# Optimization experiments

Hardware: AMD Instinct MI355X
Metric: run time of the kernel (lower is better)

The kernel has to match this reference:

```python
import jax, jax.numpy as jnp
import numpy as np

V, D, H, L, DF = 32000, 768, 12, 12, 3072
B, S, BS = 2, 1024, 16
MASK_ID = V - 1
HD = D // H
STD = 0.02


def setup_inputs() -> dict:
    key = jax.random.key(0)
    ks = jax.random.split(key, 12)
    ids = jax.random.randint(ks[0], (B, S), 0, V)
    m = jax.random.uniform(ks[1], (B, S)) < 0.15
    input_ids = jnp.where(m, MASK_ID, ids)
    target_ids = jax.random.randint(ks[2], (B, S), 0, V)
    noise_level = jax.random.uniform(ks[3], (B,), minval=0.1, maxval=1.0)
    emb = jax.random.normal(ks[4], (V, D)) * STD
    in_w = jax.random.normal(ks[5], (L, 3 * D, D)) * STD
    in_b = jnp.zeros((L, 3 * D))
    attn_out_w = jax.random.normal(ks[6], (L, D, D)) * STD
    attn_out_b = jnp.zeros((L, D))
    ln1_w = jnp.ones((L, D)); ln1_b = jnp.zeros((L, D))
    ln2_w = jnp.ones((L, D)); ln2_b = jnp.zeros((L, D))
    w1 = jax.random.normal(ks[7], (L, DF, D)) * STD; b1 = jnp.zeros((L, DF))
    w2 = jax.random.normal(ks[8], (L, D, DF)) * STD; b2 = jnp.zeros((L, D))
    proj_w = jax.random.normal(ks[9], (V, D)) * STD; proj_b = jnp.zeros((V,))
    return dict(input_ids=input_ids, target_ids=target_ids, noise_level=noise_level,
                emb=emb, in_w=in_w, in_b=in_b, attn_out_w=attn_out_w, attn_out_b=attn_out_b,
                ln1_w=ln1_w, ln1_b=ln1_b, ln2_w=ln2_w, ln2_b=ln2_b,
                w1=w1, b1=b1, w2=w2, b2=b2, proj_w=proj_w, proj_b=proj_b)


def _ln(x, w, b):
    m = x.mean(-1, keepdims=True)
    v = ((x - m) ** 2).mean(-1, keepdims=True)
    return (x - m) / jnp.sqrt(v + 1e-5) * w + b


def _rotary(x):
    # Vectorized equivalent of the per-scalar torch loop: rotates pairs
    # (0,1),(2,3),... within the first rotary_dim = D//2 channels only.
    rd = D // 2
    freqs = 1.0 / (10000.0 ** (jnp.arange(0, rd, 2, dtype=jnp.float32) / rd))  # [rd//2]
    ang = jnp.arange(S, dtype=jnp.float32)[:, None] * freqs[None, :]           # [S, rd//2]
    cos, sin = jnp.cos(ang), jnp.sin(ang)
    xr = x[..., :rd].reshape(B, S, rd // 2, 2)
    x0, x1 = xr[..., 0], xr[..., 1]
    r0 = x0 * cos - x1 * sin
    r1 = x0 * sin + x1 * cos
    rot = jnp.stack([r0, r1], axis=-1).reshape(B, S, rd)
    return jnp.concatenate([rot, x[..., rd:]], axis=-1)


def _block_causal_mask():
    nb = S // BS
    bm = jnp.tril(jnp.ones((nb, nb), dtype=jnp.float32))
    em = jnp.repeat(jnp.repeat(bm, BS, axis=0), BS, axis=1)  # [S, S]
    return (1.0 - em) * -1e9


def _model(input_ids, target_ids, noise_level, emb, in_w, in_b, attn_out_w, attn_out_b,
           ln1_w, ln1_b, ln2_w, ln2_b, w1, b1, w2, b2, proj_w, proj_b):
    x = emb[input_ids]                 # [B, S, D]
    x = _rotary(x)
    mask = _block_causal_mask()        # [S, S] additive
    scale = 1.0 / jnp.sqrt(jnp.float32(HD))
    for l in range(L):
        h = _ln(x, ln1_w[l], ln1_b[l])
        qkv = h @ in_w[l].T + in_b[l]
        q, k, v = jnp.split(qkv, 3, axis=-1)
        q = q.reshape(B, S, H, HD).transpose(0, 2, 1, 3)
        k = k.reshape(B, S, H, HD).transpose(0, 2, 1, 3)
        v = v.reshape(B, S, H, HD).transpose(0, 2, 1, 3)
        scores = jnp.einsum('bhqd,bhkd->bhqk', q, k) * scale + mask
        a = jax.nn.softmax(scores, axis=-1)
        o = jnp.einsum('bhqk,bhkd->bhqd', a, v).transpose(0, 2, 1, 3).reshape(B, S, D)
        x = x + (o @ attn_out_w[l].T + attn_out_b[l])
        h = _ln(x, ln2_w[l], ln2_b[l])
        x = x + (jax.nn.gelu(h @ w1[l].T + b1[l], approximate=False) @ w2[l].T + b2[l])
    logits = x @ proj_w.T + proj_b     # [B, S, V]
    logp = jax.nn.log_softmax(logits, axis=-1)
    ce = -jnp.take_along_axis(logp, target_ids[..., None], axis=-1)[..., 0]  # [B, S]
    is_masked = (input_ids == MASK_ID).astype(logits.dtype)
    weighted = ce * is_masked / noise_level[:, None]
    loss = weighted.sum() / (is_masked.sum() + 1e-8)
    return loss, logits


def reference(input_ids, target_ids, noise_level, emb, in_w, in_b, attn_out_w, attn_out_b,
              ln1_w, ln1_b, ln2_w, ln2_b, w1, b1, w2, b2, proj_w, proj_b):
    return _model(input_ids, target_ids, noise_level, emb, in_w, in_b, attn_out_w, attn_out_b,
                  ln1_w, ln1_b, ln2_w, ln2_b, w1, b1, w2, b2, proj_w, proj_b)
```

## Files before the change

### kernel.cpp

```cpp
#include <hip/hip_runtime.h>
#include <hip/hip_bf16.h>
#include <math.h>

#define V_SZ 32000
#define D_SZ 768
#define H_SZ 12
#define L_SZ 12
#define DF_SZ 3072
#define B_SZ 2
#define S_SZ 1024
#define BS_SZ 16
#define HD_SZ 64
#define MASK_ID 31999
#define NTOK (B_SZ * S_SZ)

typedef __attribute__((ext_vector_type(8))) short bf16x8;
typedef __attribute__((ext_vector_type(4))) short bf16x4;
typedef __attribute__((ext_vector_type(4))) float f32x4;

union B8 { bf16x8 v; __hip_bfloat162 h[4]; };
union B4 { bf16x4 v; __hip_bfloat162 h[2]; };
union U4 { ushort4 u; __hip_bfloat162 h[2]; };
union U4E { ushort4 u; unsigned short e[4]; };

__device__ inline unsigned short f2bf(float x) {
    __hip_bfloat16 b = __float2bfloat16(x);
    union { __hip_bfloat16 b; unsigned short u; } c; c.b = b;
    return c.u;
}

__global__ __launch_bounds__(256) void conv_fold_kernel(
    const float* __restrict__ Wsrc, const float* __restrict__ lnw,
    const float* __restrict__ lnb, const float* __restrict__ bsrc,
    unsigned short* __restrict__ Wdst, float* __restrict__ bdst,
    int rows_per_layer)
{
    const int gw = (blockIdx.x * 256 + threadIdx.x) >> 6;
    const int lane = threadIdx.x & 63;
    const int l = gw / rows_per_layer;
    const float* src = Wsrc + (size_t)gw * D_SZ;
    const float* wv = lnw + l * D_SZ;
    const float* bv = lnb + l * D_SZ;
    unsigned short* dst = Wdst + (size_t)gw * D_SZ;
    float acc = 0.f;
#pragma unroll
    for (int j = 0; j < 3; ++j) {
        int k = lane * 4 + j * 256;
        float4 s = *(const float4*)(src + k);
        float4 w = *(const float4*)(wv + k);
        float4 bb = *(const float4*)(bv + k);
        acc += bb.x * s.x + bb.y * s.y + bb.z * s.z + bb.w * s.w;
        U4 o;
        o.h[0] = __float22bfloat162_rn(float2{s.x * w.x, s.y * w.y});
        o.h[1] = __float22bfloat162_rn(float2{s.z * w.z, s.w * w.w});
        *(ushort4*)(dst + k) = o.u;
    }
#pragma unroll
    for (int off = 32; off; off >>= 1) acc += __shfl_xor(acc, off);
    if (lane == 0) bdst[gw] = bsrc[gw] + acc;
}

__global__ __launch_bounds__(256) void conv_cast_kernel(
    const float* __restrict__ src, unsigned short* __restrict__ dst, int n8)
{
    int i = blockIdx.x * 256 + threadIdx.x;
    if (i >= n8) return;
    const float* p = src + (size_t)i * 8;
    float4 v0 = *(const float4*)p;
    float4 v1 = *(const float4*)(p + 4);
    B8 r;
    r.h[0] = __float22bfloat162_rn(float2{v0.x, v0.y});
    r.h[1] = __float22bfloat162_rn(float2{v0.z, v0.w});
    r.h[2] = __float22bfloat162_rn(float2{v1.x, v1.y});
    r.h[3] = __float22bfloat162_rn(float2{v1.z, v1.w});
    *(bf16x8*)(dst + (size_t)i * 8) = r.v;
}

__global__ __launch_bounds__(256) void embed_rot_kernel(
    const int* __restrict__ ids, const float* __restrict__ emb,
    float* __restrict__ x)
{
    const int tok = blockIdx.x;
    const int s = tok & (S_SZ - 1);
    const int id = ids[tok];
    const float* e = emb + (size_t)id * D_SZ;
    float* xo = x + (size_t)tok * D_SZ;
    const int t = threadIdx.x;

    if (t < 192) {
        float x0 = e[2 * t], x1 = e[2 * t + 1];
        float freq = powf(10000.f, -((float)(2 * t)) / 384.f);
        float ang = (float)s * freq;
        float sn, cs;
        sincosf(ang, &sn, &cs);
        xo[2 * t]     = x0 * cs - x1 * sn;
        xo[2 * t + 1] = x0 * sn + x1 * cs;
    }
    for (int ch = 384 + t; ch < D_SZ; ch += 256) xo[ch] = e[ch];
}

template<int BM, int BN, int AM, int CM, bool WB16, bool XSWZ, bool CEP>
__global__ __launch_bounds__(256) void mfma_gemm(
    const void* __restrict__ Av, const void* __restrict__ Wv,
    const float* __restrict__ bias, const float* __restrict__ Res,
    float* __restrict__ C,
    unsigned short* __restrict__ qp, unsigned short* __restrict__ kp,
    unsigned short* __restrict__ vp, float2* __restrict__ pm,
    int M, int N, int K)
{
    constexpr int LDST = 48;
    constexpr int MR = BM / 32;
    constexpr int NR = BN / 32;
    constexpr int ACH = BM * 4 / 256;
    constexpr int BCH = BN * 4 / 256;

    __shared__ __align__(16) unsigned short As[2][BM * LDST];
    __shared__ __align__(16) unsigned short Bs[2][BN * LDST];
    __shared__ float smean[AM == 1 ? BM : 1];
    __shared__ float srstd[AM == 1 ? BM : 1];

    const int tid = threadIdx.x;
    const int lane = tid & 63;
    const int wave = tid >> 6;
    const int wrow0 = (wave >> 1) * (BM / 2);
    const int wcol0 = (wave & 1) * (BN / 2);
    const int kgrp = lane >> 4;
    const int rc = lane & 15;

    int m0, n0;
    if constexpr (XSWZ) {
        int nwg = gridDim.x * gridDim.y;
        int id = blockIdx.y * gridDim.x + blockIdx.x;
        int cpx = nwg >> 3;
        int swz = (id & 7) * cpx + (id >> 3);
        m0 = (swz % gridDim.x) * BM;
        n0 = (swz / gridDim.x) * BN;
    } else {
        m0 = blockIdx.x * BM;
        n0 = blockIdx.y * BN;
    }

    if constexpr (AM == 1) {
        const float* A = (const float*)Av;
        const int row = tid >> 2, q = tid & 3;
        const float* xr = A + (size_t)(m0 + row) * K + q * (K >> 2);
        float sum = 0.f, ss = 0.f;
        for (int j = 0; j < (K >> 4); ++j) {
            float4 v = *(const float4*)(xr + j * 4);
            sum += v.x + v.y + v.z + v.w;
            ss += v.x * v.x + v.y * v.y + v.z * v.z + v.w * v.w;
        }
        sum += __shfl_xor(sum, 1); sum += __shfl_xor(sum, 2);
        ss  += __shfl_xor(ss, 1);  ss  += __shfl_xor(ss, 2);
        float mean = sum * (1.f / (float)K);
        float var = ss * (1.f / (float)K) - mean * mean;
        if (q == 0) { smean[row] = mean; srstd[row] = rsqrtf(var + 1e-5f); }
        __syncthreads();
    }

    f32x4 acc[MR][NR];
#pragma unroll
    for (int i = 0; i < MR; ++i)
#pragma unroll
        for (int j = 0; j < NR; ++j) acc[i][j] = (f32x4){0.f, 0.f, 0.f, 0.f};

    float areg_0[AM != 2 ? ACH : 1][8], areg_1[AM != 2 ? ACH : 1][8];
    bf16x8 areg16_0[AM == 2 ? ACH : 1], areg16_1[AM == 2 ? ACH : 1];
    float bregf_0[WB16 ? 1 : BCH][8], bregf_1[WB16 ? 1 : BCH][8];
    bf16x8 breg16_0[WB16 ? BCH : 1], breg16_1[WB16 ? BCH : 1];

#define STAGE_LOAD(ST, K0) do {                                              \
    const int k0_ = (K0);                                                    \
    _Pragma("unroll")                                                        \
    for (int i_ = 0; i_ < ACH; ++i_) {                                       \
        int c_ = tid + i_ * 256;                                             \
        int row_ = c_ >> 2, ks_ = c_ & 3;                                    \
        if constexpr (AM == 2) {                                             \
            const unsigned short* A16_ = (const unsigned short*)Av;          \
            areg16_##ST[i_] = *(const bf16x8*)(A16_ + (size_t)(m0 + row_) * K + k0_ + ks_ * 8); \
        } else {                                                             \
            const float* Af_ = (const float*)Av;                             \
            const float* p_ = Af_ + (size_t)(m0 + row_) * K + k0_ + ks_ * 8; \
            float4 v0_ = *(const float4*)p_;                                 \
            float4 v1_ = *(const float4*)(p_ + 4);                           \
            areg_##ST[i_][0] = v0_.x; areg_##ST[i_][1] = v0_.y;              \
            areg_##ST[i_][2] = v0_.z; areg_##ST[i_][3] = v0_.w;              \
            areg_##ST[i_][4] = v1_.x; areg_##ST[i_][5] = v1_.y;              \
            areg_##ST[i_][6] = v1_.z; areg_##ST[i_][7] = v1_.w;              \
        }                                                                    \
    }                                                                        \
    _Pragma("unroll")                                                        \
    for (int i_ = 0; i_ < BCH; ++i_) {                                       \
        int c_ = tid + i_ * 256;                                             \
        int row_ = c_ >> 2, ks_ = c_ & 3;                                    \
        if constexpr (WB16) {                                                \
            const unsigned short* W16_ = (const unsigned short*)Wv;          \
            breg16_##ST[i_] = *(const bf16x8*)(W16_ + (size_t)(n0 + row_) * K + k0_ + ks_ * 8); \
        } else {                                                             \
            const float* Wf_ = (const float*)Wv;                             \
            const float* p_ = Wf_ + (size_t)(n0 + row_) * K + k0_ + ks_ * 8; \
            float4 v0_ = *(const float4*)p_;                                 \
            float4 v1_ = *(const float4*)(p_ + 4);                           \
            bregf_##ST[i_][0] = v0_.x; bregf_##ST[i_][1] = v0_.y;            \
            bregf_##ST[i_][2] = v0_.z; bregf_##ST[i_][3] = v0_.w;            \
            bregf_##ST[i_][4] = v1_.x; bregf_##ST[i_][5] = v1_.y;            \
            bregf_##ST[i_][6] = v1_.z; bregf_##ST[i_][7] = v1_.w;            \
        }                                                                    \
    }                                                                        \
} while (0)

#define STAGE_WRITE(ST, BUF) do {                                            \
    _Pragma("unroll")                                                        \
    for (int i_ = 0; i_ < ACH; ++i_) {                                       \
        int c_ = tid + i_ * 256;                                             \
        int row_ = c_ >> 2, ks_ = c_ & 3;                                    \
        if constexpr (AM == 2) {                                             \
            *(bf16x8*)&As[BUF][row_ * LDST + ks_ * 8] = areg16_##ST[i_];     \
        } else {                                                             \
            float sc_ = 1.f, sh_ = 0.f;                                      \
            if constexpr (AM == 1) { sc_ = srstd[row_]; sh_ = -smean[row_] * sc_; } \
            B8 r_;                                                           \
            r_.h[0] = __float22bfloat162_rn(float2{fmaf(areg_##ST[i_][0], sc_, sh_), fmaf(areg_##ST[i_][1], sc_, sh_)}); \
            r_.h[1] = __float22bfloat162_rn(float2{fmaf(areg_##ST[i_][2], sc_, sh_), fmaf(areg_##ST[i_][3], sc_, sh_)}); \
            r_.h[2] = __float22bfloat162_rn(float2{fmaf(areg_##ST[i_][4], sc_, sh_), fmaf(areg_##ST[i_][5], sc_, sh_)}); \
            r_.h[3] = __float22bfloat162_rn(float2{fmaf(areg_##ST[i_][6], sc_, sh_), fmaf(areg_##ST[i_][7], sc_, sh_)}); \
            *(bf16x8*)&As[BUF][row_ * LDST + ks_ * 8] = r_.v;                \
        }                                                                    \
    }                                                                        \
    _Pragma("unroll")                                                        \
    for (int i_ = 0; i_ < BCH; ++i_) {                                       \
        int c_ = tid + i_ * 256;                                             \
        int row_ = c_ >> 2, ks_ = c_ & 3;                                    \
        if constexpr (WB16) {                                                \
            *(bf16x8*)&Bs[BUF][row_ * LDST + ks_ * 8] = breg16_##ST[i_];     \
        } else {                                                             \
            B8 r_;                                                           \
            r_.h[0] = __float22bfloat162_rn(float2{bregf_##ST[i_][0], bregf_##ST[i_][1]}); \
            r_.h[1] = __float22bfloat162_rn(float2{bregf_##ST[i_][2], bregf_##ST[i_][3]}); \
            r_.h[2] = __float22bfloat162_rn(float2{bregf_##ST[i_][4], bregf_##ST[i_][5]}); \
            r_.h[3] = __float22bfloat162_rn(float2{bregf_##ST[i_][6], bregf_##ST[i_][7]}); \
            *(bf16x8*)&Bs[BUF][row_ * LDST + ks_ * 8] = r_.v;                \
        }                                                                    \
    }                                                                        \
} while (0)

#define COMPUTE(BUF) do {                                                    \
    bf16x8 af_[MR], bf_[NR];                                                 \
    _Pragma("unroll")                                                        \
    for (int mi_ = 0; mi_ < MR; ++mi_)                                       \
        af_[mi_] = *(const bf16x8*)&As[BUF][(wrow0 + mi_ * 16 + rc) * LDST + kgrp * 8]; \
    _Pragma("unroll")                                                        \
    for (int ni_ = 0; ni_ < NR; ++ni_)                                       \
        bf_[ni_] = *(const bf16x8*)&Bs[BUF][(wcol0 + ni_ * 16 + rc) * LDST + kgrp * 8]; \
    _Pragma("unroll")                                                        \
    for (int mi_ = 0; mi_ < MR; ++mi_)                                       \
        _Pragma("unroll")                                                    \
        for (int ni_ = 0; ni_ < NR; ++ni_)                                   \
            acc[mi_][ni_] = __builtin_amdgcn_mfma_f32_16x16x32_bf16(         \
                af_[mi_], bf_[ni_], acc[mi_][ni_], 0, 0, 0);                 \
} while (0)

    const int nk = K >> 5;
    STAGE_LOAD(0, 0);
    STAGE_WRITE(0, 0);
    STAGE_LOAD(0, 32);
    __syncthreads();

    for (int s2 = 0; s2 < nk; s2 += 2) {
        if (s2 + 2 < nk) STAGE_LOAD(1, (s2 + 2) << 5);
        COMPUTE(0);
        if (s2 + 1 < nk) STAGE_WRITE(0, 1);
        __syncthreads();
        if (s2 + 3 < nk) STAGE_LOAD(0, (s2 + 3) << 5);
        COMPUTE(1);
        if (s2 + 2 < nk) STAGE_WRITE(1, 0);
        __syncthreads();
    }
#undef STAGE_LOAD
#undef STAGE_WRITE
#undef COMPUTE

#pragma unroll
    for (int mi = 0; mi < MR; ++mi) {
#pragma unroll
        for (int ni = 0; ni < NR; ++ni) {
            const int col = n0 + wcol0 + ni * 16 + rc;
            const int rbase = m0 + wrow0 + mi * 16 + kgrp * 4;
            float bv = bias ? bias[col] : 0.f;
            if constexpr (CM == 1) {
                const int region = col / 768;
                const int c768 = col - region * 768;
                const int hh = c768 >> 6, d = c768 & 63;
                const int bb = rbase >> 10, s0 = rbase & 1023;
                const int bh = bb * H_SZ + hh;
                if (region == 0) {
#pragma unroll
                    for (int i = 0; i < 4; ++i)
                        qp[((size_t)(bh << 10) + s0 + i) * 64 + d]
                            = f2bf((acc[mi][ni][i] + bv) * 0.125f);
                } else if (region == 1) {
#pragma unroll
                    for (int i = 0; i < 4; ++i)
                        kp[((size_t)(bh << 10) + s0 + i) * 64 + d]
                            = f2bf(acc[mi][ni][i] + bv);
                } else {
                    U4E t4;
#pragma unroll
                    for (int i = 0; i < 4; ++i) t4.e[i] = f2bf(acc[mi][ni][i] + bv);
                    *(ushort4*)&vp[(((size_t)bh * 64 + d) << 10) + s0] = t4.u;
                }
            } else if constexpr (CM == 2) {
                unsigned short* C16 = (unsigned short*)C;
#pragma unroll
                for (int i = 0; i < 4; ++i) {
                    float v = acc[mi][ni][i] + bv;
                    v = 0.5f * v * (1.f + erff(v * 0.70710678118654752f));
                    C16[(size_t)(rbase + i) * N + col] = f2bf(v);
                }
            } else {
                size_t basei = (size_t)rbase * N + col;
#pragma unroll
                for (int i = 0; i < 4; ++i) {
                    float v = acc[mi][ni][i] + bv;
                    size_t idx = basei + (size_t)i * N;
                    if (Res) v += Res[idx];
                    C[idx] = v;
                }
            }
        }
    }

    if constexpr (CEP) {
        float2 (*sce)[2] = (float2 (*)[2])As;
        float bvv[NR];
#pragma unroll
        for (int ni = 0; ni < NR; ++ni) bvv[ni] = bias[n0 + wcol0 + ni * 16 + rc];
#pragma unroll
        for (int mi = 0; mi < MR; ++mi) {
#pragma unroll
            for (int i = 0; i < 4; ++i) {
                float vmax = -1e30f;
#pragma unroll
                for (int ni = 0; ni < NR; ++ni)
                    vmax = fmaxf(vmax, acc[mi][ni][i] + bvv[ni]);
                vmax = fmaxf(vmax, __shfl_xor(vmax, 1));
                vmax = fmaxf(vmax, __shfl_xor(vmax, 2));
                vmax = fmaxf(vmax, __shfl_xor(vmax, 4));
                vmax = fmaxf(vmax, __shfl_xor(vmax, 8));
                float ssum = 0.f;
#pragma unroll
                for (int ni = 0; ni < NR; ++ni)
                    ssum += __expf(acc[mi][ni][i] + bvv[ni] - vmax);
                ssum += __shfl_xor(ssum, 1);
                ssum += __shfl_xor(ssum, 2);
                ssum += __shfl_xor(ssum, 4);
                ssum += __shfl_xor(ssum, 8);
                if (rc == 0)
                    sce[wrow0 + mi * 16 + kgrp * 4 + i][wave & 1] = float2{vmax, ssum};
            }
        }
        __syncthreads();
        if (tid < BM) {
            float2 a = sce[tid][0], b2 = sce[tid][1];
            float Mv = fmaxf(a.x, b2.x);
            float Sv = a.y * __expf(a.x - Mv) + b2.y * __expf(b2.x - Mv);
            pm[(size_t)(n0 >> 7) * NTOK + m0 + tid] = float2{Mv, Sv};
        }
    }
}

__global__ __launch_bounds__(256) void attn3_kernel(
    const unsigned short* __restrict__ Q16, const unsigned short* __restrict__ K16,
    const unsigned short* __restrict__ VT16, unsigned short* __restrict__ ao16)
{
    const int bid = blockIdx.x;
    const int qb = 63 - bid / 24;
    const int bh = bid % 24;
    const int b = bh / H_SZ, h = bh % H_SZ;
    const int tid = threadIdx.x;
    const int w = tid >> 6, lane = tid & 63;
    const int g = lane >> 4, r = lane & 15;

    constexpr int KS = 72;
    __shared__ __align__(16) unsigned short Pl[4][16 * KS];
    __shared__ float so[4][16][66];
    __shared__ float2 sml[4][16];

    const unsigned short* Qb = Q16 + ((size_t)bh << 10) * 64;
    const unsigned short* Kb = K16 + ((size_t)bh << 10) * 64;
    const unsigned short* Vb = VT16 + ((size_t)bh << 6) * 1024;

    bf16x8 qf[2];
    qf[0] = *(const bf16x8*)&Qb[(qb * 16 + r) * 64 + 8 * g];
    qf[1] = *(const bf16x8*)&Qb[(qb * 16 + r) * 64 + 32 + 8 * g];

    float m_r = -1e30f, l_r = 0.f;
    f32x4 o[4];
#pragma unroll
    for (int ni = 0; ni < 4; ++ni) o[ni] = (f32x4){0.f, 0.f, 0.f, 0.f};

    const int nch = (qb >> 2) + 1;
    const int qbm = qb & 3;

    for (int c = w; c < nch; c += 4) {
        const bool lastc = (c == nch - 1);
        const int mi_hi = lastc ? qbm : 3;

        f32x4 s[4];
#pragma unroll
        for (int mi = 0; mi < 4; ++mi) s[mi] = (f32x4){0.f, 0.f, 0.f, 0.f};
#pragma unroll
        for (int mi = 0; mi < 4; ++mi) {
            if (mi <= mi_hi) {
#pragma unroll
                for (int ks = 0; ks < 2; ++ks) {
                    bf16x8 af = *(const bf16x8*)&Kb[(c * 64 + 16 * mi + r) * 64 + 32 * ks + 8 * g];
                    s[mi] = __builtin_amdgcn_mfma_f32_16x16x32_bf16(af, qf[ks], s[mi], 0, 0, 0);
                }
            }
        }

        float mx = -1e30f;
#pragma unroll
        for (int mi = 0; mi < 4; ++mi) {
            if (mi <= mi_hi) {
#pragma unroll
                for (int i = 0; i < 4; ++i) mx = fmaxf(mx, s[mi][i]);
            }
        }
        mx = fmaxf(mx, __shfl_xor(mx, 16));
        mx = fmaxf(mx, __shfl_xor(mx, 32));
        float m_new = fmaxf(m_r, mx);
        float corr = __expf(m_r - m_new);

        float p[4][4];
        float psum = 0.f;
#pragma unroll
        for (int mi = 0; mi < 4; ++mi) {
#pragma unroll
            for (int i = 0; i < 4; ++i) {
                float pv = (mi <= mi_hi) ? __expf(s[mi][i] - m_new) : 0.f;
                p[mi][i] = pv;
                psum += pv;
            }
        }
        psum += __shfl_xor(psum, 16);
        psum += __shfl_xor(psum, 32);
        l_r = l_r * corr + psum;
        m_r = m_new;

#pragma unroll
        for (int mi = 0; mi < 4; ++mi) {
            B4 t;
            t.h[0] = __float22bfloat162_rn(float2{p[mi][0], p[mi][1]});
            t.h[1] = __float22bfloat162_rn(float2{p[mi][2], p[mi][3]});
            *(bf16x4*)&Pl[w][r * KS + 16 * mi + 4 * g] = t.v;
        }

        float co[4];
#pragma unroll
        for (int i = 0; i < 4; ++i) co[i] = __shfl(corr, 4 * g + i);
#pragma unroll
        for (int ni = 0; ni < 4; ++ni)
#pragma unroll
            for (int i = 0; i < 4; ++i) o[ni][i] *= co[i];

#pragma unroll
        for (int ks = 0; ks < 2; ++ks) {
            if (!lastc || 2 * ks <= qbm) {
                bf16x8 pf = *(const bf16x8*)&Pl[w][r * KS + 32 * ks + 8 * g];
#pragma unroll
                for (int ni = 0; ni < 4; ++ni) {
                    bf16x8 vf = *(const bf16x8*)&Vb[(size_t)(r + 16 * ni) * 1024 + c * 64 + 32 * ks + 8 * g];
                    o[ni] = __builtin_amdgcn_mfma_f32_16x16x32_bf16(pf, vf, o[ni], 0, 0, 0);
                }
            }
        }
    }

    if (g == 0) sml[w][r] = float2{m_r, l_r};
#pragma unroll
    for (int ni = 0; ni < 4; ++ni)
#pragma unroll
        for (int i = 0; i < 4; ++i)
            so[w][4 * g + i][r + 16 * ni] = o[ni][i];
    __syncthreads();

#pragma unroll
    for (int j = 0; j < 4; ++j) {
        int e = tid + j * 256;
        int row = e >> 6, col = e & 63;
        float2 p0 = sml[0][row], p1 = sml[1][row], p2 = sml[2][row], p3 = sml[3][row];
        float M = fmaxf(fmaxf(p0.x, p1.x), fmaxf(p2.x, p3.x));
        float w0 = __expf(p0.x - M), w1 = __expf(p1.x - M);
        float w2 = __expf(p2.x - M), w3 = __expf(p3.x - M);
        float L = p0.y * w0 + p1.y * w1 + p2.y * w2 + p3.y * w3;
        float ov = so[0][row][col] * w0 + so[1][row][col] * w1
                 + so[2][row][col] * w2 + so[3][row][col] * w3;
        ao16[(size_t)(b * S_SZ + qb * 16 + row) * D_SZ + h * HD_SZ + col]
            = f2bf(ov / L);
    }
}

__global__ __launch_bounds__(256) void ce2_kernel(
    const float* __restrict__ logits, const int* __restrict__ tgt,
    const int* __restrict__ inp, const float* __restrict__ noise,
    float* __restrict__ ce_row, float* __restrict__ msk_row)
{
    const int row = blockIdx.x;
    const int t = threadIdx.x;
    const float* lr = logits + (size_t)row * V_SZ;
    const float4* lr4 = (const float4*)lr;

    float m = -1e30f, s = 0.f;
    for (int i = t; i < V_SZ / 4; i += 256) {
        float4 v = lr4[i];
        float mx4 = fmaxf(fmaxf(v.x, v.y), fmaxf(v.z, v.w));
        if (mx4 > m) { s *= __expf(m - mx4); m = mx4; }
        s += __expf(v.x - m) + __expf(v.y - m) + __expf(v.z - m) + __expf(v.w - m);
    }

    __shared__ float sm[256], ss[256];
    sm[t] = m; ss[t] = s;
    __syncthreads();
    for (int off = 128; off; off >>= 1) {
        if (t < off) {
            float m2 = fmaxf(sm[t], sm[t + off]);
            ss[t] = ss[t] * __expf(sm[t] - m2) + ss[t + off] * __expf(sm[t + off] - m2);
            sm[t] = m2;
        }
        __syncthreads();
    }
    if (t == 0) {
        float M = sm[0], S = ss[0];
        int tg = tgt[row];
        float ce = -(lr[tg] - M - logf(S));
        int ism = (inp[row] == MASK_ID) ? 1 : 0;
        int b = row / S_SZ;
        ce_row[row] = ism ? (ce / noise[b]) : 0.f;
        msk_row[row] = ism ? 1.f : 0.f;
    }
}

__global__ __launch_bounds__(64) void ce3_kernel(
    const float2* __restrict__ pm, const float* __restrict__ logits,
    const int* __restrict__ tgt, const int* __restrict__ inp,
    const float* __restrict__ noise, float* __restrict__ ce_row,
    float* __restrict__ msk_row)
{
    const int row = blockIdx.x * 64 + threadIdx.x;
    float m = -1e30f, s = 0.f;
    for (int bb = 0; bb < V_SZ / 128; ++bb) {
        float2 p = pm[(size_t)bb * NTOK + row];
        float M2 = fmaxf(m, p.x);
        s = s * __expf(m - M2) + p.y * __expf(p.x - M2);
        m = M2;
    }
    int tg = tgt[row];
    float lv = logits[(size_t)row * V_SZ + tg];
    float ce = -(lv - m - logf(s));
    int ism = (inp[row] == MASK_ID) ? 1 : 0;
    int b = row / S_SZ;
    ce_row[row] = ism ? (ce / noise[b]) : 0.f;
    msk_row[row] = ism ? 1.f : 0.f;
}

__global__ __launch_bounds__(256) void loss_reduce_kernel(
    const float* __restrict__ ce_row, const float* __restrict__ msk_row,
    float* __restrict__ out0)
{
    const int t = threadIdx.x;
    __shared__ float r1[256], r2[256];
    float s = 0.f, c = 0.f;
    for (int i = t; i < NTOK; i += 256) { s += ce_row[i]; c += msk_row[i]; }
    r1[t] = s; r2[t] = c;
    __syncthreads();
    for (int off = 128; off; off >>= 1) {
        if (t < off) { r1[t] += r1[t + off]; r2[t] += r2[t + off]; }
        __syncthreads();
    }
    if (t == 0) out0[0] = r1[0] / (r2[0] + 1e-8f);
}

extern "C" void kernel_launch(void* const* d_in, const int* in_sizes, int n_in,
                              void* d_out, int out_size, void* d_ws, size_t ws_size,
                              hipStream_t stream)
{
    const int*   input_ids  = (const int*)d_in[0];
    const int*   target_ids = (const int*)d_in[1];
    const float* noise      = (const float*)d_in[2];
    const float* emb        = (const float*)d_in[3];
    const float* in_w       = (const float*)d_in[4];
    const float* in_b       = (const float*)d_in[5];
    const float* aow        = (const float*)d_in[6];
    const float* aob        = (const float*)d_in[7];
    const float* ln1w       = (const float*)d_in[8];
    const float* ln1b       = (const float*)d_in[9];
    const float* ln2w       = (const float*)d_in[10];
    const float* ln2b       = (const float*)d_in[11];
    const float* w1         = (const float*)d_in[12];
    const float* b1         = (const float*)d_in[13];
    const float* w2         = (const float*)d_in[14];
    const float* b2         = (const float*)d_in[15];
    const float* projw      = (const float*)d_in[16];
    const float* projb      = (const float*)d_in[17];

    float* out    = (float*)d_out;
    float* logits = out + 1;

    float* base = out + 4;
    unsigned short* wq16 = (unsigned short*)(base);
    unsigned short* wa16 = (unsigned short*)(base + 10616832);
    unsigned short* w116 = (unsigned short*)(base + 14155776);
    unsigned short* w216 = (unsigned short*)(base + 28311552);
    float* qkvb2 = base + 42467328;
    float* b1b2  = qkvb2 + 27648;
    unsigned short* Q16  = (unsigned short*)(base + 42531840);
    unsigned short* K16  = (unsigned short*)(base + 43318272);
    unsigned short* VT16 = (unsigned short*)(base + 44104704);
    unsigned short* ao16 = (unsigned short*)(base + 44891136);
    unsigned short* mid16= (unsigned short*)(base + 45677568);

    float* x       = (float*)d_ws;
    float* ce_row  = x + (size_t)NTOK * D_SZ;
    float* msk_row = ce_row + NTOK;
    unsigned short* xb16 = (unsigned short*)(msk_row + NTOK);
    unsigned short* projw16 = xb16 + (size_t)NTOK * D_SZ;
    float2* pm = (float2*)d_ws;
    const bool fA = ws_size >= 9453568ull;
    const bool fB = ws_size >= 58605568ull;

    conv_fold_kernel<<<6912, 256, 0, stream>>>(in_w, ln1w, ln1b, in_b, wq16, qkvb2, 2304);
    conv_fold_kernel<<<9216, 256, 0, stream>>>(w1, ln2w, ln2b, b1, w116, b1b2, 3072);
    conv_cast_kernel<<<3456, 256, 0, stream>>>(aow, wa16, 884736);
    conv_cast_kernel<<<13824, 256, 0, stream>>>(w2, w216, 3538944);
    if (fB)
        conv_cast_kernel<<<12000, 256, 0, stream>>>(projw, projw16, 3072000);

    embed_rot_kernel<<<NTOK, 256, 0, stream>>>(input_ids, emb, x);

    for (int l = 0; l < L_SZ; ++l) {
        mfma_gemm<64, 128, 1, 1, true, false, false><<<dim3(32, 18), 256, 0, stream>>>(
            x, wq16 + (size_t)l * 1769472, qkvb2 + l * 2304, nullptr, nullptr,
            Q16, K16, VT16, nullptr, NTOK, 2304, 768);
        attn3_kernel<<<1536, 256, 0, stream>>>(Q16, K16, VT16, ao16);
        mfma_gemm<64, 64, 2, 0, true, false, false><<<dim3(32, 12), 256, 0, stream>>>(
            ao16, wa16 + (size_t)l * 589824, aob + l * D_SZ, x, x,
            nullptr, nullptr, nullptr, nullptr, NTOK, 768, 768);
        mfma_gemm<64, 128, 1, 2, true, false, false><<<dim3(32, 24), 256, 0, stream>>>(
            x, w116 + (size_t)l * 2359296, b1b2 + l * 3072, nullptr, (float*)mid16,
            nullptr, nullptr, nullptr, nullptr, NTOK, 3072, 768);
        mfma_gemm<64, 64, 2, 0, true, false, false><<<dim3(32, 12), 256, 0, stream>>>(
            mid16, w216 + (size_t)l * 2359296, b2 + l * D_SZ, x, x,
            nullptr, nullptr, nullptr, nullptr, NTOK, 768, 3072);
    }

    if (fA)
        conv_cast_kernel<<<768, 256, 0, stream>>>(x, xb16, 196608);

    if (fB) {
        mfma_gemm<128, 128, 2, 0, true, true, true><<<dim3(16, 250), 256, 0, stream>>>(
            xb16, projw16, projb, nullptr, logits,
            nullptr, nullptr, nullptr, pm, NTOK, V_SZ, 768);
        ce3_kernel<<<32, 64, 0, stream>>>(pm, logits, target_ids, input_ids,
                                          noise, ce_row, msk_row);
    } else if (fA) {
        mfma_gemm<128, 128, 2, 0, false, true, true><<<dim3(16, 250), 256, 0, stream>>>(
            xb16, projw, projb, nullptr, logits,
            nullptr, nullptr, nullptr, pm, NTOK, V_SZ, 768);
        ce3_kernel<<<32, 64, 0, stream>>>(pm, logits, target_ids, input_ids,
                                          noise, ce_row, msk_row);
    } else {
        mfma_gemm<128, 128, 0, 0, false, true, false><<<dim3(16, 250), 256, 0, stream>>>(
            x, projw, projb, nullptr, logits,
            nullptr, nullptr, nullptr, nullptr, NTOK, V_SZ, 768);
        ce2_kernel<<<NTOK, 256, 0, stream>>>(logits, target_ids, input_ids, noise,
                                             ce_row, msk_row);
    }

    loss_reduce_kernel<<<1, 256, 0, stream>>>(ce_row, msk_row, out);
}
```

Baseline: 2.669 ms.

## Load bf16 GEMM operands directly into LDS with global_load_lds

After: 2.794 ms. 1.05x slower.

```diff
diff --git a/kernel.cpp b/kernel.cpp
--- a/kernel.cpp
+++ b/kernel.cpp
@@ -29,6 +29,11 @@
     return c.u;
 }
 
+#define GLL16(G, L)                                                          \
+    __builtin_amdgcn_global_load_lds(                                       \
+        (const __attribute__((address_space(1))) void*)(G),                 \
+        (__attribute__((address_space(3))) void*)(L), 16, 0, 0)
+
 __global__ __launch_bounds__(256) void conv_fold_kernel(
     const float* __restrict__ Wsrc, const float* __restrict__ lnw,
     const float* __restrict__ lnb, const float* __restrict__ bsrc,
@@ -108,19 +113,22 @@
     unsigned short* __restrict__ vp, float2* __restrict__ pm,
     int M, int N, int K)
 {
-    constexpr int LDST = 48;
+    constexpr bool GLLA = (AM == 2);
+    constexpr int ALD = GLLA ? 32 : 48;
+    constexpr int BLD = WB16 ? 32 : 48;
     constexpr int MR = BM / 32;
     constexpr int NR = BN / 32;
     constexpr int ACH = BM * 4 / 256;
     constexpr int BCH = BN * 4 / 256;
 
-    __shared__ __align__(16) unsigned short As[2][BM * LDST];
-    __shared__ __align__(16) unsigned short Bs[2][BN * LDST];
+    __shared__ __align__(16) unsigned short As[2][BM * ALD];
+    __shared__ __align__(16) unsigned short Bs[2][BN * BLD];
     __shared__ float smean[AM == 1 ? BM : 1];
     __shared__ float srstd[AM == 1 ? BM : 1];
 
     const int tid = threadIdx.x;
     const int lane = tid & 63;
+    const int wbase = tid & 192;
     const int wave = tid >> 6;
     const int wrow0 = (wave >> 1) * (BM / 2);
     const int wcol0 = (wave & 1) * (BN / 2);
@@ -129,9 +137,8 @@
 
     int m0, n0;
     if constexpr (XSWZ) {
-        int nwg = gridDim.x * gridDim.y;
         int id = blockIdx.y * gridDim.x + blockIdx.x;
-        int cpx = nwg >> 3;
+        int cpx = (gridDim.x * gridDim.y) >> 3;
         int swz = (id & 7) * cpx + (id >> 3);
         m0 = (swz % gridDim.x) * BM;
         n0 = (swz / gridDim.x) * BN;
@@ -164,121 +171,122 @@
 #pragma unroll
         for (int j = 0; j < NR; ++j) acc[i][j] = (f32x4){0.f, 0.f, 0.f, 0.f};
 
-    float areg_0[AM != 2 ? ACH : 1][8], areg_1[AM != 2 ? ACH : 1][8];
-    bf16x8 areg16_0[AM == 2 ? ACH : 1], areg16_1[AM == 2 ? ACH : 1];
-    float bregf_0[WB16 ? 1 : BCH][8], bregf_1[WB16 ? 1 : BCH][8];
-    bf16x8 breg16_0[WB16 ? BCH : 1], breg16_1[WB16 ? BCH : 1];
-
-#define STAGE_LOAD(ST, K0) do {                                              \
-    const int k0_ = (K0);                                                    \
-    _Pragma("unroll")                                                        \
-    for (int i_ = 0; i_ < ACH; ++i_) {                                       \
-        int c_ = tid + i_ * 256;                                             \
-        int row_ = c_ >> 2, ks_ = c_ & 3;                                    \
-        if constexpr (AM == 2) {                                             \
-            const unsigned short* A16_ = (const unsigned short*)Av;          \
-            areg16_##ST[i_] = *(const bf16x8*)(A16_ + (size_t)(m0 + row_) * K + k0_ + ks_ * 8); \
-        } else {                                                             \
-            const float* Af_ = (const float*)Av;                             \
-            const float* p_ = Af_ + (size_t)(m0 + row_) * K + k0_ + ks_ * 8; \
-            float4 v0_ = *(const float4*)p_;                                 \
-            float4 v1_ = *(const float4*)(p_ + 4);                           \
-            areg_##ST[i_][0] = v0_.x; areg_##ST[i_][1] = v0_.y;              \
-            areg_##ST[i_][2] = v0_.z; areg_##ST[i_][3] = v0_.w;              \
-            areg_##ST[i_][4] = v1_.x; areg_##ST[i_][5] = v1_.y;              \
-            areg_##ST[i_][6] = v1_.z; areg_##ST[i_][7] = v1_.w;              \
-        }                                                                    \
-    }                                                                        \
-    _Pragma("unroll")                                                        \
-    for (int i_ = 0; i_ < BCH; ++i_) {                                       \
-        int c_ = tid + i_ * 256;                                             \
-        int row_ = c_ >> 2, ks_ = c_ & 3;                                    \
-        if constexpr (WB16) {                                                \
-            const unsigned short* W16_ = (const unsigned short*)Wv;          \
-            breg16_##ST[i_] = *(const bf16x8*)(W16_ + (size_t)(n0 + row_) * K + k0_ + ks_ * 8); \
-        } else {                                                             \
-            const float* Wf_ = (const float*)Wv;                             \
-            const float* p_ = Wf_ + (size_t)(n0 + row_) * K + k0_ + ks_ * 8; \
-            float4 v0_ = *(const float4*)p_;                                 \
-            float4 v1_ = *(const float4*)(p_ + 4);                           \
-            bregf_##ST[i_][0] = v0_.x; bregf_##ST[i_][1] = v0_.y;            \
-            bregf_##ST[i_][2] = v0_.z; bregf_##ST[i_][3] = v0_.w;            \
-            bregf_##ST[i_][4] = v1_.x; bregf_##ST[i_][5] = v1_.y;            \
-            bregf_##ST[i_][6] = v1_.z; bregf_##ST[i_][7] = v1_.w;            \
-        }                                                                    \
-    }                                                                        \
-} while (0)
-
-#define STAGE_WRITE(ST, BUF) do {                                            \
-    _Pragma("unroll")                                                        \
-    for (int i_ = 0; i_ < ACH; ++i_) {                                       \
-        int c_ = tid + i_ * 256;                                             \
-        int row_ = c_ >> 2, ks_ = c_ & 3;                                    \
-        if constexpr (AM == 2) {                                             \
-            *(bf16x8*)&As[BUF][row_ * LDST + ks_ * 8] = areg16_##ST[i_];     \
-        } else {                                                             \
-            float sc_ = 1.f, sh_ = 0.f;                                      \
-            if constexpr (AM == 1) { sc_ = srstd[row_]; sh_ = -smean[row_] * sc_; } \
-            B8 r_;                                                           \
-            r_.h[0] = __float22bfloat162_rn(float2{fmaf(areg_##ST[i_][0], sc_, sh_), fmaf(areg_##ST[i_][1], sc_, sh_)}); \
-            r_.h[1] = __float22bfloat162_rn(float2{fmaf(areg_##ST[i_][2], sc_, sh_), fmaf(areg_##ST[i_][3], sc_, sh_)}); \
-            r_.h[2] = __float22bfloat162_rn(float2{fmaf(areg_##ST[i_][4], sc_, sh_), fmaf(areg_##ST[i_][5], sc_, sh_)}); \
-            r_.h[3] = __float22bfloat162_rn(float2{fmaf(areg_##ST[i_][6], sc_, sh_), fmaf(areg_##ST[i_][7], sc_, sh_)}); \
-            *(bf16x8*)&As[BUF][row_ * LDST + ks_ * 8] = r_.v;                \
-        }                                                                    \
-    }                                                                        \
-    _Pragma("unroll")                                                        \
-    for (int i_ = 0; i_ < BCH; ++i_) {                                       \
-        int c_ = tid + i_ * 256;                                             \
-        int row_ = c_ >> 2, ks_ = c_ & 3;                                    \
-        if constexpr (WB16) {                                                \
-            *(bf16x8*)&Bs[BUF][row_ * LDST + ks_ * 8] = breg16_##ST[i_];     \
-        } else {                                                             \
-            B8 r_;                                                           \
-            r_.h[0] = __float22bfloat162_rn(float2{bregf_##ST[i_][0], bregf_##ST[i_][1]}); \
-            r_.h[1] = __float22bfloat162_rn(float2{bregf_##ST[i_][2], bregf_##ST[i_][3]}); \
-            r_.h[2] = __float22bfloat162_rn(float2{bregf_##ST[i_][4], bregf_##ST[i_][5]}); \
-            r_.h[3] = __float22bfloat162_rn(float2{bregf_##ST[i_][6], bregf_##ST[i_][7]}); \
-            *(bf16x8*)&Bs[BUF][row_ * LDST + ks_ * 8] = r_.v;                \
-        }                                                                    \
-    }                                                                        \
-} while (0)
-
-#define COMPUTE(BUF) do {                                                    \
-    bf16x8 af_[MR], bf_[NR];                                                 \
-    _Pragma("unroll")                                                        \
-    for (int mi_ = 0; mi_ < MR; ++mi_)                                       \
-        af_[mi_] = *(const bf16x8*)&As[BUF][(wrow0 + mi_ * 16 + rc) * LDST + kgrp * 8]; \
-    _Pragma("unroll")                                                        \
-    for (int ni_ = 0; ni_ < NR; ++ni_)                                       \
-        bf_[ni_] = *(const bf16x8*)&Bs[BUF][(wcol0 + ni_ * 16 + rc) * LDST + kgrp * 8]; \
-    _Pragma("unroll")                                                        \
-    for (int mi_ = 0; mi_ < MR; ++mi_)                                       \
-        _Pragma("unroll")                                                    \
-        for (int ni_ = 0; ni_ < NR; ++ni_)                                   \
-            acc[mi_][ni_] = __builtin_amdgcn_mfma_f32_16x16x32_bf16(         \
-                af_[mi_], bf_[ni_], acc[mi_][ni_], 0, 0, 0);                 \
-} while (0)
+    float areg[(AM != 2) ? ACH : 1][8];
+    float bregf[WB16 ? 1 : BCH][8];
+
+    auto gll_a = [&](int buf, int k0) {
+        const unsigned short* A16 = (const unsigned short*)Av;
+#pragma unroll
+        for (int i = 0; i < ACH; ++i) {
+            int c = tid + i * 256;
+            int row = c >> 2, ks = c & 3;
+            GLL16(A16 + (size_t)(m0 + row) * K + k0 + ks * 8,
+                  &As[buf][(i * 256 + wbase) * 8]);
+        }
+    };
+    auto load_a = [&](int k0) {
+#pragma unroll
+        for (int i = 0; i < ACH; ++i) {
+            int c = tid + i * 256;
+            int row = c >> 2, ks = c & 3;
+            const float* p = (const float*)Av + (size_t)(m0 + row) * K + k0 + ks * 8;
+            float4 v0 = *(const float4*)p;
+            float4 v1 = *(const float4*)(p + 4);
+            areg[i][0] = v0.x; areg[i][1] = v0.y; areg[i][2] = v0.z; areg[i][3] = v0.w;
+            areg[i][4] = v1.x; areg[i][5] = v1.y; areg[i][6] = v1.z; areg[i][7] = v1.w;
+        }
+    };
+    auto write_a = [&](int buf) {
+#pragma unroll
+        for (int i = 0; i < ACH; ++i) {
+            int c = tid + i * 256;
+            int row = c >> 2, ks = c & 3;
+            float sc = 1.f, sh = 0.f;
+            if constexpr (AM == 1) { sc = srstd[row]; sh = -smean[row] * sc; }
+            B8 r;
+            r.h[0] = __float22bfloat162_rn(float2{fmaf(areg[i][0], sc, sh), fmaf(areg[i][1], sc, sh)});
+            r.h[1] = __float22bfloat162_rn(float2{fmaf(areg[i][2], sc, sh), fmaf(areg[i][3], sc, sh)});
+            r.h[2] = __float22bfloat162_rn(float2{fmaf(areg[i][4], sc, sh), fmaf(areg[i][5], sc, sh)});
+            r.h[3] = __float22bfloat162_rn(float2{fmaf(areg[i][6], sc, sh), fmaf(areg[i][7], sc, sh)});
+            *(bf16x8*)&As[buf][row * ALD + ks * 8] = r.v;
+        }
+    };
+
+    auto gll_b = [&](int buf, int k0) {
+        const unsigned short* W16 = (const unsigned short*)Wv;
+#pragma unroll
+        for (int i = 0; i < BCH; ++i) {
+            int c = tid + i * 256;
+            int row = c >> 2, ks = c & 3;
+            GLL16(W16 + (size_t)(n0 + row) * K + k0 + ks * 8,
+                  &Bs[buf][(i * 256 + wbase) * 8]);
+        }
+    };
+    auto load_b = [&](int k0) {
+#pragma unroll
+        for (int i = 0; i < BCH; ++i) {
+            int c = tid + i * 256;
+            int row = c >> 2, ks = c & 3;
+            const float* p = (const float*)Wv + (size_t)(n0 + row) * K + k0 + ks * 8;
+            float4 v0 = *(const float4*)p;
+            float4 v1 = *(const float4*)(p + 4);
+            bregf[i][0] = v0.x; bregf[i][1] = v0.y; bregf[i][2] = v0.z; bregf[i][3] = v0.w;
+            bregf[i][4] = v1.x; bregf[i][5] = v1.y; bregf[i][6] = v1.z; bregf[i][7] = v1.w;
+        }
+    };
+    auto write_b = [&](int buf) {
+#pragma unroll
+        for (int i = 0; i < BCH; ++i) {
+            int c = tid + i * 256;
+            int row = c >> 2, ks = c & 3;
+            B8 r;
+            r.h[0] = __float22bfloat162_rn(float2{bregf[i][0], bregf[i][1]});
+            r.h[1] = __float22bfloat162_rn(float2{bregf[i][2], bregf[i][3]});
+            r.h[2] = __float22bfloat162_rn(float2{bregf[i][4], bregf[i][5]});
+            r.h[3] = __float22bfloat162_rn(float2{bregf[i][6], bregf[i][7]});
+            *(bf16x8*)&Bs[buf][row * BLD + ks * 8] = r.v;
+        }
+    };
+
+    auto compute = [&](int buf) {
+        bf16x8 af[MR], bf[NR];
+#pragma unroll
+        for (int mi = 0; mi < MR; ++mi)
+            af[mi] = *(const bf16x8*)&As[buf][(wrow0 + mi * 16 + rc) * ALD + kgrp * 8];
+#pragma unroll
+        for (int ni = 0; ni < NR; ++ni)
+            bf[ni] = *(const bf16x8*)&Bs[buf][(wcol0 + ni * 16 + rc) * BLD + kgrp * 8];
+#pragma unroll
+        for (int mi = 0; mi < MR; ++mi)
+#pragma unroll
+            for (int ni = 0; ni < NR; ++ni)
+                acc[mi][ni] = __builtin_amdgcn_mfma_f32_16x16x32_bf16(
+                    af[mi], bf[ni], acc[mi][ni], 0, 0, 0);
+    };
+
+    if constexpr (GLLA) gll_a(0, 0); else load_a(0);
+    if constexpr (WB16) gll_b(0, 0); else load_b(0);
+    if constexpr (!GLLA) write_a(0);
+    if constexpr (!WB16) write_b(0);
+    __syncthreads();
 
     const int nk = K >> 5;
-    STAGE_LOAD(0, 0);
-    STAGE_WRITE(0, 0);
-    STAGE_LOAD(0, 32);
-    __syncthreads();
-
-    for (int s2 = 0; s2 < nk; s2 += 2) {
-        if (s2 + 2 < nk) STAGE_LOAD(1, (s2 + 2) << 5);
-        COMPUTE(0);
-        if (s2 + 1 < nk) STAGE_WRITE(0, 1);
+    int cur = 0;
+    for (int s = 0; s < nk; ++s) {
+        const bool more = (s + 1 < nk);
+        const int k1 = (s + 1) << 5;
+        if (more) {
+            if constexpr (GLLA) gll_a(cur ^ 1, k1); else load_a(k1);
+            if constexpr (WB16) gll_b(cur ^ 1, k1); else load_b(k1);
+        }
+        compute(cur);
+        if (more) {
+            if constexpr (!GLLA) write_a(cur ^ 1);
+            if constexpr (!WB16) write_b(cur ^ 1);
+        }
         __syncthreads();
-        if (s2 + 3 < nk) STAGE_LOAD(0, (s2 + 3) << 5);
-        COMPUTE(1);
-        if (s2 + 2 < nk) STAGE_WRITE(1, 0);
-        __syncthreads();
-    }
-#undef STAGE_LOAD
-#undef STAGE_WRITE
-#undef COMPUTE
+        cur ^= 1;
+    }
 
 #pragma unroll
     for (int mi = 0; mi < MR; ++mi) {
```
